# Performance work log

Measured on AMD Instinct MI355X. Metric: run time of the kernel, lower is better.

The kernel has to match this reference:

```python
import jax, jax.numpy as jnp
import numpy as np

ROI = 7      # pooled output size
S = 5        # max adaptive samples per bin dim (boxes <= 0.25*120=30px -> ceil(30/7)=5)


def _roi_align(f, boxes):
    """torchvision roi_align, aligned=True, sampling_ratio=-1 (adaptive).
    f: [C,H,W]; boxes: [N,4] normalized xywh. Returns [N,C,ROI,ROI]."""
    C, H, W = f.shape
    fH, fW = jnp.float32(H), jnp.float32(W)
    x1 = boxes[:, 0] * fW - 0.5                 # aligned=True offset
    y1 = boxes[:, 1] * fH - 0.5
    roi_w = boxes[:, 2] * fW
    roi_h = boxes[:, 3] * fH
    bin_w = roi_w / ROI
    bin_h = roi_h / ROI
    gw = jnp.maximum(jnp.ceil(roi_w / ROI), 1.0)   # adaptive grid counts [N]
    gh = jnp.maximum(jnp.ceil(roi_h / ROI), 1.0)
    ph = jnp.arange(ROI, dtype=jnp.float32)
    s = jnp.arange(S, dtype=jnp.float32)
    # sample coords [N, ROI, S]
    ys = y1[:, None, None] + ph[None, :, None] * bin_h[:, None, None] \
         + (s[None, None, :] + 0.5) * bin_h[:, None, None] / gh[:, None, None]
    xs = x1[:, None, None] + ph[None, :, None] * bin_w[:, None, None] \
         + (s[None, None, :] + 0.5) * bin_w[:, None, None] / gw[:, None, None]
    # broadcast to [N, ROI, ROI, S, S]
    y = ys[:, :, None, :, None]
    x = xs[:, None, :, None, :]
    m = ((s[None, None, None, :, None] < gh[:, None, None, None, None]) &
         (s[None, None, None, None, :] < gw[:, None, None, None, None]))
    valid = (y > -1.0) & (y < fH) & (x > -1.0) & (x < fW)
    yc = jnp.clip(y, 0.0, fH - 1.0)
    xc = jnp.clip(x, 0.0, fW - 1.0)
    y0 = jnp.floor(yc).astype(jnp.int32)
    x0 = jnp.floor(xc).astype(jnp.int32)
    yh = jnp.minimum(y0 + 1, H - 1)
    xh = jnp.minimum(x0 + 1, W - 1)
    ly = yc - y0.astype(jnp.float32); hy = 1.0 - ly
    lx = xc - x0.astype(jnp.float32); hx = 1.0 - lx
    scale = (valid & m).astype(f.dtype)
    y = jnp.broadcast_to(y0 * 0, (boxes.shape[0], ROI, ROI, S, S))  # shape anchor (unused)
    w00 = (hy * hx * scale)[None]
    w01 = (hy * lx * scale)[None]
    w10 = (ly * hx * scale)[None]
    w11 = (ly * lx * scale)[None]
    # gathered values: [C, N, ROI, ROI, S, S]
    vals = (w00 * f[:, y0, x0] + w01 * f[:, y0, xh] +
            w10 * f[:, yh, x0] + w11 * f[:, yh, xh])
    count = (gh * gw)[None, :, None, None]
    pooled = vals.sum(axis=(-1, -2)) / count        # [C, N, ROI, ROI]
    return pooled.transpose(1, 0, 2, 3)              # [N, C, ROI, ROI]


def setup_inputs() -> dict:
    key = jax.random.key(0)
    k = jax.random.split(key, 6)
    features = jax.random.normal(k[0], (1, 128, 120, 120), jnp.float32)
    u = jax.random.uniform(k[1], (512, 4), jnp.float32)
    boxes = jnp.stack([u[:, 0] * 0.7, u[:, 1] * 0.7,
                       0.05 + 0.2 * u[:, 2], 0.05 + 0.2 * u[:, 3]], axis=1)
    d_in = 128 * ROI * ROI  # 6272
    W1 = jax.random.normal(k[2], (d_in, 512), jnp.float32) / np.float32(np.sqrt(d_in))
    b1 = jax.random.normal(k[3], (512,), jnp.float32) * 0.01
    W2 = jax.random.normal(k[4], (512, 256), jnp.float32) / np.float32(np.sqrt(512))
    b2 = jax.random.normal(k[5], (256,), jnp.float32) * 0.01
    return {"features": features, "boxes": boxes, "W1": W1, "b1": b1, "W2": W2, "b2": b2}


def reference(features, boxes, W1, b1, W2, b2):
    roi = _roi_align(features[0], boxes)             # [N,128,7,7]
    flat = roi.reshape(roi.shape[0], -1)             # [N,6272] channel-major like torch .view
    h = jax.nn.relu(flat @ W1 + b1)                  # dropout in eval mode = identity
    return h @ W2 + b2                               # [N,256]
```

## Files before the change

### kernel.cpp

```cpp
#include <hip/hip_runtime.h>
#include <hip/hip_bf16.h>
#include <stdint.h>

#define DI __device__ __forceinline__

typedef __attribute__((ext_vector_type(8))) short short8;
typedef __attribute__((ext_vector_type(4))) float f32x4;

constexpr int CH   = 128;
constexpr int FH   = 120;
constexpr int FW   = 120;
constexpr int NBOX = 512;
constexpr int KDIM = 49 * 128;
constexpr int D1   = 512;
constexpr int D2   = 256;
constexpr int SPLITS = 14;
constexpr int KC     = KDIM / SPLITS;

DI float bf2f(uint32_t u16) { union { uint32_t i; float f; } v; v.i = u16 << 16; return v.f; }
DI uint16_t f2bf(float f) {
    __hip_bfloat16 h = __float2bfloat16(f);
    union { __hip_bfloat16 h; uint16_t u; } v; v.h = h; return v.u;
}

__global__ __launch_bounds__(256) void k_pre(const float* __restrict__ f,
                                             const float* __restrict__ W1,
                                             const float* __restrict__ W2,
                                             uint32_t* __restrict__ ft,
                                             uint16_t* __restrict__ W1rT,
                                             uint16_t* __restrict__ W2T) {
    __shared__ __align__(16) char smem[16896];
    const int v = blockIdx.x, t = threadIdx.x;
    if (v < 480) {
        float* lds = (float*)smem;
        const int y = v >> 2, x0 = (v & 3) * 30;
        for (int e = t; e < 30 * 128; e += 256) {
            int c = e / 30, x = e - c * 30;
            lds[x * 129 + c] = f[c * (FH * FW) + y * FW + x0 + x];
        }
        __syncthreads();
        for (int e = t; e < 30 * 64; e += 256) {
            int x = e >> 6, cp = e & 63;
            float lo = lds[x * 129 + 2 * cp];
            float hi = lds[x * 129 + 2 * cp + 1];
            ft[(y * FW + x0 + x) * 64 + cp] = (uint32_t)f2bf(lo) | ((uint32_t)f2bf(hi) << 16);
        }
    } else if (v < 512) {
        float* lds = (float*)smem;
        const int v2 = v - 480;
        const int n0 = (v2 & 7) * 32, k0 = (v2 >> 3) * 128;
        for (int e = t; e < 4096; e += 256) {
            int k = e >> 5, nn = e & 31;
            lds[k * 33 + nn] = W2[(k0 + k) * D2 + n0 + nn];
        }
        __syncthreads();
        for (int e = t; e < 4096; e += 256) {
            int nn = e >> 7, k = e & 127;
            W2T[(n0 + nn) * D1 + k0 + k] = f2bf(lds[k * 33 + nn]);
        }
    } else {
        float* lds = (float*)smem;
        const int vb = v - 512;
        const int b = vb % 49, j0 = (vb / 49) * 32;
        for (int e = t; e < 4096; e += 256) {
            int ci = e >> 5, jj = e & 31;
            lds[ci * 33 + jj] = W1[(ci * 49 + b) * D1 + j0 + jj];
        }
        __syncthreads();
        for (int e = t; e < 4096; e += 256) {
            int jj = e >> 7, ci = e & 127;
            W1rT[(size_t)(j0 + jj) * KDIM + b * 128 + ci] = f2bf(lds[ci * 33 + jj]);
        }
    }
}

__global__ __launch_bounds__(256) void k_roi(const uint32_t* __restrict__ ft,
                                             const float* __restrict__ boxes,
                                             uint32_t* __restrict__ A) {
#pragma clang fp contract(off)
    const int wid  = (blockIdx.x << 2) + (threadIdx.x >> 6);
    const int lane = threadIdx.x & 63;
    const int box = wid / 49, bin = wid % 49;
    const int ph = bin / 7, pw = bin % 7;

    const float bx = boxes[box * 4 + 0], by = boxes[box * 4 + 1];
    const float bw = boxes[box * 4 + 2], bh = boxes[box * 4 + 3];
    const float x1 = bx * 120.0f - 0.5f;
    const float y1 = by * 120.0f - 0.5f;
    const float roi_w = bw * 120.0f, roi_h = bh * 120.0f;
    const float bin_w = roi_w / 7.0f, bin_h = roi_h / 7.0f;
    const float gwf = fmaxf(ceilf(roi_w / 7.0f), 1.0f);
    const float ghf = fmaxf(ceilf(roi_h / 7.0f), 1.0f);
    const int gwi = (int)gwf, ghi = (int)ghf;

    const float ybase = y1 + (float)ph * bin_h;
    const float xbase = x1 + (float)pw * bin_w;

    float acc0 = 0.0f, acc1 = 0.0f;
    for (int sy = 0; sy < ghi; ++sy) {
        float yy = ybase + ((float)sy + 0.5f) * bin_h / ghf;
        bool vy = (yy > -1.0f) && (yy < 120.0f);
        float yc = fminf(fmaxf(yy, 0.0f), 119.0f);
        int y0 = (int)floorf(yc);
        int yh = min(y0 + 1, 119);
        float ly = yc - (float)y0, hy = 1.0f - ly;
        const uint32_t* r0 = ft + (size_t)(y0 * FW) * 64;
        const uint32_t* r1 = ft + (size_t)(yh * FW) * 64;
        for (int sx = 0; sx < gwi; ++sx) {
            float xx = xbase + ((float)sx + 0.5f) * bin_w / gwf;
            if (!(vy && (xx > -1.0f) && (xx < 120.0f))) continue;
            float xc = fminf(fmaxf(xx, 0.0f), 119.0f);
            int x0 = (int)floorf(xc);
            int xh = min(x0 + 1, 119);
            float lx = xc - (float)x0, hx = 1.0f - lx;
            float w00 = hy * hx, w01 = hy * lx, w10 = ly * hx, w11 = ly * lx;
            uint32_t u00 = r0[x0 * 64 + lane];
            uint32_t u01 = r0[xh * 64 + lane];
            uint32_t u10 = r1[x0 * 64 + lane];
            uint32_t u11 = r1[xh * 64 + lane];
            acc0 += w00 * bf2f(u00 & 0xffffu) + w01 * bf2f(u01 & 0xffffu)
                  + w10 * bf2f(u10 & 0xffffu) + w11 * bf2f(u11 & 0xffffu);
            acc1 += w00 * bf2f(u00 >> 16) + w01 * bf2f(u01 >> 16)
                  + w10 * bf2f(u10 >> 16) + w11 * bf2f(u11 >> 16);
        }
    }
    const float cnt = ghf * gwf;
    const float v0 = acc0 / cnt, v1 = acc1 / cnt;
    A[(size_t)wid * 64 + lane] = (uint32_t)f2bf(v0) | ((uint32_t)f2bf(v1) << 16);
}

__global__ __launch_bounds__(256) void k_gemm1(const uint16_t* __restrict__ A,
                                               const uint16_t* __restrict__ B,
                                               float* __restrict__ P) {
    __shared__ __align__(16) uint16_t As[128 * 32];
    __shared__ __align__(16) uint16_t Bs[128 * 32];
    const int t = threadIdx.x;
    const int lane = t & 63, w = t >> 6;
    const int wr = w >> 1, wc = w & 1;
    const int m0 = blockIdx.x * 128, n0 = blockIdx.y * 128;
    const int kbase = blockIdx.z * KC;

    f32x4 acc[4][4] = {};
    const int kb = lane >> 4, r16 = lane & 15;

    for (int ks = 0; ks < KC / 32; ++ks) {
        const int kk = kbase + ks * 32;
        __syncthreads();
#pragma unroll
        for (int i = 0; i < 2; ++i) {
            int ch = t + 256 * i;
            int row = ch >> 2, c8 = ch & 3;
            int sw = (row >> 1) & 3;
            const uint16_t* ga = A + (size_t)(m0 + row) * KDIM + kk + c8 * 8;
            *(uint4*)&As[row * 32 + (c8 ^ sw) * 8] = *(const uint4*)ga;
            const uint16_t* gb = B + (size_t)(n0 + row) * KDIM + kk + c8 * 8;
            *(uint4*)&Bs[row * 32 + (c8 ^ sw) * 8] = *(const uint4*)gb;
        }
        __syncthreads();

        short8 af[4], bfr[4];
#pragma unroll
        for (int mi = 0; mi < 4; ++mi) {
            int ar = wr * 64 + mi * 16 + r16;
            af[mi] = *(const short8*)&As[ar * 32 + (kb ^ ((ar >> 1) & 3)) * 8];
        }
#pragma unroll
        for (int ni = 0; ni < 4; ++ni) {
            int br = wc * 64 + ni * 16 + r16;
            bfr[ni] = *(const short8*)&Bs[br * 32 + (kb ^ ((br >> 1) & 3)) * 8];
        }
#pragma unroll
        for (int mi = 0; mi < 4; ++mi)
#pragma unroll
            for (int ni = 0; ni < 4; ++ni)
                acc[mi][ni] = __builtin_amdgcn_mfma_f32_16x16x32_bf16(af[mi], bfr[ni], acc[mi][ni], 0, 0, 0);
    }

    float* outp = P + (size_t)blockIdx.z * (D1 * D1);
#pragma unroll
    for (int mi = 0; mi < 4; ++mi)
#pragma unroll
        for (int ni = 0; ni < 4; ++ni) {
            int row = m0 + wr * 64 + mi * 16 + kb * 4;
            int col = n0 + wc * 64 + ni * 16 + r16;
#pragma unroll
            for (int r = 0; r < 4; ++r)
                outp[(size_t)(row + r) * D1 + col] = acc[mi][ni][r];
        }
}

__global__ __launch_bounds__(256) void k_reduce1(const float* __restrict__ P,
                                                 const float* __restrict__ b1,
                                                 uint16_t* __restrict__ Hm) {
    const int e4 = blockIdx.x * 256 + threadIdx.x;
    const f32x4* P4 = (const f32x4*)P;
    f32x4 s = {};
#pragma unroll
    for (int i = 0; i < SPLITS; ++i) s += P4[(size_t)i * (D1 * D1 / 4) + e4];
    const int c4 = (e4 & 127) * 4;
    uint16_t h[4];
#pragma unroll
    for (int j = 0; j < 4; ++j) h[j] = f2bf(fmaxf(s[j] + b1[c4 + j], 0.0f));
    uint2 pk;
    pk.x = (uint32_t)h[0] | ((uint32_t)h[1] << 16);
    pk.y = (uint32_t)h[2] | ((uint32_t)h[3] << 16);
    *(uint2*)&Hm[(size_t)e4 * 4] = pk;
}

__global__ __launch_bounds__(256) void k_gemm2(const uint16_t* __restrict__ Hm,
                                               const uint16_t* __restrict__ W2T,
                                               const float* __restrict__ b2,
                                               float* __restrict__ out) {
    const int wid  = blockIdx.x * 4 + (threadIdx.x >> 6);
    const int lane = threadIdx.x & 63;
    const int mt = wid >> 4, nt = wid & 15;
    const int m0 = mt * 16, n0 = nt * 16;
    const int g = lane >> 4, i = lane & 15;
    f32x4 acc = {};
#pragma unroll
    for (int kk = 0; kk < D1 / 32; ++kk) {
        short8 a = *(const short8*)&Hm[(m0 + i) * D1 + kk * 32 + g * 8];
        short8 b = *(const short8*)&W2T[(n0 + i) * D1 + kk * 32 + g * 8];
        acc = __builtin_amdgcn_mfma_f32_16x16x32_bf16(a, b, acc, 0, 0, 0);
    }
    const float bias = b2[n0 + i];
#pragma unroll
    for (int r = 0; r < 4; ++r)
        out[(size_t)(m0 + g * 4 + r) * D2 + n0 + i] = acc[r] + bias;
}

extern "C" void kernel_launch(void* const* d_in, const int* in_sizes, int n_in,
                              void* d_out, int out_size, void* d_ws, size_t ws_size,
                              hipStream_t stream) {
    const float* f     = (const float*)d_in[0];
    const float* boxes = (const float*)d_in[1];
    const float* W1    = (const float*)d_in[2];
    const float* b1    = (const float*)d_in[3];
    const float* W2    = (const float*)d_in[4];
    const float* b2    = (const float*)d_in[5];
    float* out = (float*)d_out;

    char* p = (char*)d_ws;
    uint32_t* ft   = (uint32_t*)p; p += (size_t)FH * FW * (CH / 2) * 4;
    uint16_t* W1rT = (uint16_t*)p; p += (size_t)D1 * KDIM * 2;
    uint16_t* W2T  = (uint16_t*)p; p += (size_t)D2 * D1 * 2;
    uint16_t* Ar   = (uint16_t*)p; p += (size_t)NBOX * KDIM * 2;
    float*    Pp   = (float*)p;    p += (size_t)SPLITS * D1 * D1 * 4;
    uint16_t* Hm   = (uint16_t*)p; p += (size_t)D1 * D1 * 2;

    k_pre<<<1296, 256, 0, stream>>>(f, W1, W2, ft, W1rT, W2T);
    k_roi<<<(NBOX * 49) / 4, 256, 0, stream>>>(ft, boxes, (uint32_t*)Ar);
    k_gemm1<<<dim3(4, 4, SPLITS), 256, 0, stream>>>(Ar, W1rT, Pp);
    k_reduce1<<<D1 * D1 / 4 / 256, 256, 0, stream>>>(Pp, b1, Hm);
    k_gemm2<<<(D1 / 16) * (D2 / 16) / 4, 256, 0, stream>>>(Hm, W2T, b2, out);
}
```

Before: 72.96 us.

## Replace split-K partial buffers with atomic accumulation and restructure ROI sampling loop

gemm1 now accumulates its split-K partials straight into a single fp32 buffer with relaxed atomics. That buffer is zeroed by extra blocks in the preprocessing kernel. The separate reduce kernel is removed, and bias plus ReLU plus bf16 conversion are folded into gemm2's A-load. The ROI kernel also precomputes per-column x offsets and masked weights, then issues all 20 gathers per row unrolled and branch-free instead of a data-dependent inner loop. This cuts one launch and the 14-way partial-sum write/read traffic, at the cost of atomic contention, nondeterministic summation order, and extra loads for masked-out samples.

After: 81.47 us. 11.7% more time.

```diff
diff --git a/kernel.cpp b/kernel.cpp
--- a/kernel.cpp
+++ b/kernel.cpp
@@ -18,6 +18,7 @@
 constexpr int KC     = KDIM / SPLITS;
 
 DI float bf2f(uint32_t u16) { union { uint32_t i; float f; } v; v.i = u16 << 16; return v.f; }
+DI float bf2f_hi(uint32_t u) { union { uint32_t i; float f; } v; v.i = u & 0xffff0000u; return v.f; }
 DI uint16_t f2bf(float f) {
     __hip_bfloat16 h = __float2bfloat16(f);
     union { __hip_bfloat16 h; uint16_t u; } v; v.h = h; return v.u;
@@ -28,7 +29,8 @@
                                              const float* __restrict__ W2,
                                              uint32_t* __restrict__ ft,
                                              uint16_t* __restrict__ W1rT,
-                                             uint16_t* __restrict__ W2T) {
+                                             uint16_t* __restrict__ W2T,
+                                             float* __restrict__ Hf) {
     __shared__ __align__(16) char smem[16896];
     const int v = blockIdx.x, t = threadIdx.x;
     if (v < 480) {
@@ -58,7 +60,7 @@
             int nn = e >> 7, k = e & 127;
             W2T[(n0 + nn) * D1 + k0 + k] = f2bf(lds[k * 33 + nn]);
         }
-    } else {
+    } else if (v < 1296) {
         float* lds = (float*)smem;
         const int vb = v - 512;
         const int b = vb % 49, j0 = (vb / 49) * 32;
@@ -71,6 +73,11 @@
             int jj = e >> 7, ci = e & 127;
             W1rT[(size_t)(j0 + jj) * KDIM + b * 128 + ci] = f2bf(lds[ci * 33 + jj]);
         }
+    } else {
+        const int vz = v - 1296;
+        f32x4* Z = (f32x4*)(Hf + (size_t)vz * 4096);
+#pragma unroll
+        for (int i = 0; i < 4; ++i) Z[i * 256 + t] = f32x4{0.f, 0.f, 0.f, 0.f};
     }
 }
 
@@ -96,32 +103,48 @@
     const float ybase = y1 + (float)ph * bin_h;
     const float xbase = x1 + (float)pw * bin_w;
 
+    int offx0[5], offxh[5];
+    float hxm[5], lxm[5];
+#pragma unroll
+    for (int j = 0; j < 5; ++j) {
+        float xx = xbase + ((float)j + 0.5f) * bin_w / gwf;
+        bool vx = (j < gwi) && (xx > -1.0f) && (xx < 120.0f);
+        float xc = fminf(fmaxf(xx, 0.0f), 119.0f);
+        int x0 = (int)floorf(xc);
+        int xh = min(x0 + 1, 119);
+        float lx = xc - (float)x0, hx = 1.0f - lx;
+        float mx = vx ? 1.0f : 0.0f;
+        hxm[j] = hx * mx; lxm[j] = lx * mx;
+        offx0[j] = x0 * 64; offxh[j] = xh * 64;
+    }
+
     float acc0 = 0.0f, acc1 = 0.0f;
     for (int sy = 0; sy < ghi; ++sy) {
         float yy = ybase + ((float)sy + 0.5f) * bin_h / ghf;
-        bool vy = (yy > -1.0f) && (yy < 120.0f);
+        float my = ((yy > -1.0f) && (yy < 120.0f)) ? 1.0f : 0.0f;
         float yc = fminf(fmaxf(yy, 0.0f), 119.0f);
         int y0 = (int)floorf(yc);
         int yh = min(y0 + 1, 119);
         float ly = yc - (float)y0, hy = 1.0f - ly;
-        const uint32_t* r0 = ft + (size_t)(y0 * FW) * 64;
-        const uint32_t* r1 = ft + (size_t)(yh * FW) * 64;
-        for (int sx = 0; sx < gwi; ++sx) {
-            float xx = xbase + ((float)sx + 0.5f) * bin_w / gwf;
-            if (!(vy && (xx > -1.0f) && (xx < 120.0f))) continue;
-            float xc = fminf(fmaxf(xx, 0.0f), 119.0f);
-            int x0 = (int)floorf(xc);
-            int xh = min(x0 + 1, 119);
-            float lx = xc - (float)x0, hx = 1.0f - lx;
-            float w00 = hy * hx, w01 = hy * lx, w10 = ly * hx, w11 = ly * lx;
-            uint32_t u00 = r0[x0 * 64 + lane];
-            uint32_t u01 = r0[xh * 64 + lane];
-            uint32_t u10 = r1[x0 * 64 + lane];
-            uint32_t u11 = r1[xh * 64 + lane];
-            acc0 += w00 * bf2f(u00 & 0xffffu) + w01 * bf2f(u01 & 0xffffu)
-                  + w10 * bf2f(u10 & 0xffffu) + w11 * bf2f(u11 & 0xffffu);
-            acc1 += w00 * bf2f(u00 >> 16) + w01 * bf2f(u01 >> 16)
-                  + w10 * bf2f(u10 >> 16) + w11 * bf2f(u11 >> 16);
+        float hym = hy * my, lym = ly * my;
+        const uint32_t* r0 = ft + (size_t)(y0 * FW) * 64 + lane;
+        const uint32_t* r1 = ft + (size_t)(yh * FW) * 64 + lane;
+        uint32_t u00[5], u01[5], u10[5], u11[5];
+#pragma unroll
+        for (int j = 0; j < 5; ++j) {
+            u00[j] = r0[offx0[j]];
+            u01[j] = r0[offxh[j]];
+            u10[j] = r1[offx0[j]];
+            u11[j] = r1[offxh[j]];
+        }
+#pragma unroll
+        for (int j = 0; j < 5; ++j) {
+            float w00 = hym * hxm[j], w01 = hym * lxm[j];
+            float w10 = lym * hxm[j], w11 = lym * lxm[j];
+            acc0 += w00 * bf2f(u00[j] & 0xffffu) + w01 * bf2f(u01[j] & 0xffffu)
+                  + w10 * bf2f(u10[j] & 0xffffu) + w11 * bf2f(u11[j] & 0xffffu);
+            acc1 += w00 * bf2f_hi(u00[j]) + w01 * bf2f_hi(u01[j])
+                  + w10 * bf2f_hi(u10[j]) + w11 * bf2f_hi(u11[j]);
         }
     }
     const float cnt = ghf * gwf;
@@ -131,7 +154,7 @@
 
 __global__ __launch_bounds__(256) void k_gemm1(const uint16_t* __restrict__ A,
                                                const uint16_t* __restrict__ B,
-                                               float* __restrict__ P) {
+                                               float* __restrict__ Hf) {
     __shared__ __align__(16) uint16_t As[128 * 32];
     __shared__ __align__(16) uint16_t Bs[128 * 32];
     const int t = threadIdx.x;
@@ -176,7 +199,6 @@
                 acc[mi][ni] = __builtin_amdgcn_mfma_f32_16x16x32_bf16(af[mi], bfr[ni], acc[mi][ni], 0, 0, 0);
     }
 
-    float* outp = P + (size_t)blockIdx.z * (D1 * D1);
 #pragma unroll
     for (int mi = 0; mi < 4; ++mi)
 #pragma unroll
@@ -185,30 +207,15 @@
             int col = n0 + wc * 64 + ni * 16 + r16;
 #pragma unroll
             for (int r = 0; r < 4; ++r)
-                outp[(size_t)(row + r) * D1 + col] = acc[mi][ni][r];
-        }
-}
-
-__global__ __launch_bounds__(256) void k_reduce1(const float* __restrict__ P,
-                                                 const float* __restrict__ b1,
-                                                 uint16_t* __restrict__ Hm) {
-    const int e4 = blockIdx.x * 256 + threadIdx.x;
-    const f32x4* P4 = (const f32x4*)P;
-    f32x4 s = {};
-#pragma unroll
-    for (int i = 0; i < SPLITS; ++i) s += P4[(size_t)i * (D1 * D1 / 4) + e4];
-    const int c4 = (e4 & 127) * 4;
-    uint16_t h[4];
-#pragma unroll
-    for (int j = 0; j < 4; ++j) h[j] = f2bf(fmaxf(s[j] + b1[c4 + j], 0.0f));
-    uint2 pk;
-    pk.x = (uint32_t)h[0] | ((uint32_t)h[1] << 16);
-    pk.y = (uint32_t)h[2] | ((uint32_t)h[3] << 16);
-    *(uint2*)&Hm[(size_t)e4 * 4] = pk;
-}
-
-__global__ __launch_bounds__(256) void k_gemm2(const uint16_t* __restrict__ Hm,
+                __hip_atomic_fetch_add(&Hf[(size_t)(row + r) * D1 + col],
+                                       acc[mi][ni][r],
+                                       __ATOMIC_RELAXED, __HIP_MEMORY_SCOPE_AGENT);
+        }
+}
+
+__global__ __launch_bounds__(256) void k_gemm2(const float* __restrict__ Hf,
                                                const uint16_t* __restrict__ W2T,
+                                               const float* __restrict__ b1,
                                                const float* __restrict__ b2,
                                                float* __restrict__ out) {
     const int wid  = blockIdx.x * 4 + (threadIdx.x >> 6);
@@ -219,7 +226,18 @@
     f32x4 acc = {};
 #pragma unroll
     for (int kk = 0; kk < D1 / 32; ++kk) {
-        short8 a = *(const short8*)&Hm[(m0 + i) * D1 + kk * 32 + g * 8];
+        const float* hp = &Hf[(size_t)(m0 + i) * D1 + kk * 32 + g * 8];
+        f32x4 h0 = *(const f32x4*)hp;
+        f32x4 h1 = *(const f32x4*)(hp + 4);
+        const float* bp = &b1[kk * 32 + g * 8];
+        f32x4 c0 = *(const f32x4*)bp;
+        f32x4 c1 = *(const f32x4*)(bp + 4);
+        short8 a;
+#pragma unroll
+        for (int r = 0; r < 4; ++r) {
+            a[r]     = (short)f2bf(fmaxf(h0[r] + c0[r], 0.0f));
+            a[4 + r] = (short)f2bf(fmaxf(h1[r] + c1[r], 0.0f));
+        }
         short8 b = *(const short8*)&W2T[(n0 + i) * D1 + kk * 32 + g * 8];
         acc = __builtin_amdgcn_mfma_f32_16x16x32_bf16(a, b, acc, 0, 0, 0);
     }
@@ -245,12 +263,10 @@
     uint16_t* W1rT = (uint16_t*)p; p += (size_t)D1 * KDIM * 2;
     uint16_t* W2T  = (uint16_t*)p; p += (size_t)D2 * D1 * 2;
     uint16_t* Ar   = (uint16_t*)p; p += (size_t)NBOX * KDIM * 2;
-    float*    Pp   = (float*)p;    p += (size_t)SPLITS * D1 * D1 * 4;
-    uint16_t* Hm   = (uint16_t*)p; p += (size_t)D1 * D1 * 2;
-
-    k_pre<<<1296, 256, 0, stream>>>(f, W1, W2, ft, W1rT, W2T);
+    float*    Hf   = (float*)p;    p += (size_t)D1 * D1 * 4;
+
+    k_pre<<<1360, 256, 0, stream>>>(f, W1, W2, ft, W1rT, W2T, Hf);
     k_roi<<<(NBOX * 49) / 4, 256, 0, stream>>>(ft, boxes, (uint32_t*)Ar);
-    k_gemm1<<<dim3(4, 4, SPLITS), 256, 0, stream>>>(Ar, W1rT, Pp);
-    k_reduce1<<<D1 * D1 / 4 / 256, 256, 0, stream>>>(Pp, b1, Hm);
-    k_gemm2<<<(D1 / 16) * (D2 / 16) / 4, 256, 0, stream>>>(Hm, W2T, b2, out);
-}
+    k_gemm1<<<dim3(4, 4, SPLITS), 256, 0, stream>>>(Ar, W1rT, Hf);
+    k_gemm2<<<(D1 / 16) * (D2 / 16) / 4, 256, 0, stream>>>(Hf, W2T, b1, b2, out);
+}
```

## Fuse weight conversion into ROI kernel and precompute per-box sample tables

Applied to the files above, without the earlier changes.

The feature transpose now runs alone in a small pre-kernel. The W1/W2 bf16 transposes move into the ROI kernel as extra blocks, so the weight conversion overlaps with ROI pooling instead of running before it. ROI pooling now uses one 512-thread block per box: it precomputes the y/x sample offsets and bilinear weights into LDS once, and each wave handles bins using those tables. This removes redundant per-bin coordinate math, but block sizes become heterogeneous and the per-box work is less balanced.

New measurement: 91.09 us. 24.9% more time.

```diff
diff --git a/kernel.cpp b/kernel.cpp
--- a/kernel.cpp
+++ b/kernel.cpp
@@ -18,115 +18,135 @@
 constexpr int KC     = KDIM / SPLITS;
 
 DI float bf2f(uint32_t u16) { union { uint32_t i; float f; } v; v.i = u16 << 16; return v.f; }
+DI float bf2f_hi(uint32_t u) { union { uint32_t i; float f; } v; v.i = u & 0xffff0000u; return v.f; }
 DI uint16_t f2bf(float f) {
     __hip_bfloat16 h = __float2bfloat16(f);
     union { __hip_bfloat16 h; uint16_t u; } v; v.h = h; return v.u;
 }
 
-__global__ __launch_bounds__(256) void k_pre(const float* __restrict__ f,
-                                             const float* __restrict__ W1,
-                                             const float* __restrict__ W2,
-                                             uint32_t* __restrict__ ft,
-                                             uint16_t* __restrict__ W1rT,
-                                             uint16_t* __restrict__ W2T) {
-    __shared__ __align__(16) char smem[16896];
+__global__ __launch_bounds__(256) void k_preft(const float* __restrict__ f,
+                                               uint32_t* __restrict__ ft) {
+    __shared__ float lds[30 * 129];
     const int v = blockIdx.x, t = threadIdx.x;
-    if (v < 480) {
-        float* lds = (float*)smem;
-        const int y = v >> 2, x0 = (v & 3) * 30;
-        for (int e = t; e < 30 * 128; e += 256) {
-            int c = e / 30, x = e - c * 30;
-            lds[x * 129 + c] = f[c * (FH * FW) + y * FW + x0 + x];
-        }
-        __syncthreads();
-        for (int e = t; e < 30 * 64; e += 256) {
-            int x = e >> 6, cp = e & 63;
-            float lo = lds[x * 129 + 2 * cp];
-            float hi = lds[x * 129 + 2 * cp + 1];
-            ft[(y * FW + x0 + x) * 64 + cp] = (uint32_t)f2bf(lo) | ((uint32_t)f2bf(hi) << 16);
-        }
-    } else if (v < 512) {
-        float* lds = (float*)smem;
-        const int v2 = v - 480;
-        const int n0 = (v2 & 7) * 32, k0 = (v2 >> 3) * 128;
-        for (int e = t; e < 4096; e += 256) {
-            int k = e >> 5, nn = e & 31;
-            lds[k * 33 + nn] = W2[(k0 + k) * D2 + n0 + nn];
-        }
-        __syncthreads();
-        for (int e = t; e < 4096; e += 256) {
-            int nn = e >> 7, k = e & 127;
-            W2T[(n0 + nn) * D1 + k0 + k] = f2bf(lds[k * 33 + nn]);
-        }
-    } else {
-        float* lds = (float*)smem;
-        const int vb = v - 512;
-        const int b = vb % 49, j0 = (vb / 49) * 32;
-        for (int e = t; e < 4096; e += 256) {
-            int ci = e >> 5, jj = e & 31;
-            lds[ci * 33 + jj] = W1[(ci * 49 + b) * D1 + j0 + jj];
-        }
-        __syncthreads();
-        for (int e = t; e < 4096; e += 256) {
-            int jj = e >> 7, ci = e & 127;
-            W1rT[(size_t)(j0 + jj) * KDIM + b * 128 + ci] = f2bf(lds[ci * 33 + jj]);
-        }
-    }
-}
-
-__global__ __launch_bounds__(256) void k_roi(const uint32_t* __restrict__ ft,
-                                             const float* __restrict__ boxes,
-                                             uint32_t* __restrict__ A) {
+    const int y = v >> 2, x0 = (v & 3) * 30;
+    for (int e = t; e < 30 * 128; e += 256) {
+        int c = e / 30, x = e - c * 30;
+        lds[x * 129 + c] = f[c * (FH * FW) + y * FW + x0 + x];
+    }
+    __syncthreads();
+    for (int e = t; e < 30 * 64; e += 256) {
+        int x = e >> 6, cp = e & 63;
+        float lo = lds[x * 129 + 2 * cp];
+        float hi = lds[x * 129 + 2 * cp + 1];
+        ft[(y * FW + x0 + x) * 64 + cp] = (uint32_t)f2bf(lo) | ((uint32_t)f2bf(hi) << 16);
+    }
+}
+
+__global__ __launch_bounds__(512) void k_roi_w(const uint32_t* __restrict__ ft,
+                                               const float* __restrict__ boxes,
+                                               const float* __restrict__ W1,
+                                               const float* __restrict__ W2,
+                                               uint32_t* __restrict__ A,
+                                               uint16_t* __restrict__ W1rT,
+                                               uint16_t* __restrict__ W2T) {
+    __shared__ __align__(16) float lds[128 * 33];
+    __shared__ float twf[160];
+    __shared__ int   twi[160];
+    const int blk = blockIdx.x, t = threadIdx.x;
+    if (blk < 512) {
 #pragma clang fp contract(off)
-    const int wid  = (blockIdx.x << 2) + (threadIdx.x >> 6);
-    const int lane = threadIdx.x & 63;
-    const int box = wid / 49, bin = wid % 49;
-    const int ph = bin / 7, pw = bin % 7;
-
-    const float bx = boxes[box * 4 + 0], by = boxes[box * 4 + 1];
-    const float bw = boxes[box * 4 + 2], bh = boxes[box * 4 + 3];
-    const float x1 = bx * 120.0f - 0.5f;
-    const float y1 = by * 120.0f - 0.5f;
-    const float roi_w = bw * 120.0f, roi_h = bh * 120.0f;
-    const float bin_w = roi_w / 7.0f, bin_h = roi_h / 7.0f;
-    const float gwf = fmaxf(ceilf(roi_w / 7.0f), 1.0f);
-    const float ghf = fmaxf(ceilf(roi_h / 7.0f), 1.0f);
-    const int gwi = (int)gwf, ghi = (int)ghf;
-
-    const float ybase = y1 + (float)ph * bin_h;
-    const float xbase = x1 + (float)pw * bin_w;
-
-    float acc0 = 0.0f, acc1 = 0.0f;
-    for (int sy = 0; sy < ghi; ++sy) {
-        float yy = ybase + ((float)sy + 0.5f) * bin_h / ghf;
-        bool vy = (yy > -1.0f) && (yy < 120.0f);
-        float yc = fminf(fmaxf(yy, 0.0f), 119.0f);
-        int y0 = (int)floorf(yc);
-        int yh = min(y0 + 1, 119);
-        float ly = yc - (float)y0, hy = 1.0f - ly;
-        const uint32_t* r0 = ft + (size_t)(y0 * FW) * 64;
-        const uint32_t* r1 = ft + (size_t)(yh * FW) * 64;
-        for (int sx = 0; sx < gwi; ++sx) {
-            float xx = xbase + ((float)sx + 0.5f) * bin_w / gwf;
-            if (!(vy && (xx > -1.0f) && (xx < 120.0f))) continue;
+        const int box = blk;
+        const float bx = boxes[box * 4 + 0], by = boxes[box * 4 + 1];
+        const float bw = boxes[box * 4 + 2], bh = boxes[box * 4 + 3];
+        const float x1 = bx * 120.0f - 0.5f;
+        const float y1 = by * 120.0f - 0.5f;
+        const float roi_w = bw * 120.0f, roi_h = bh * 120.0f;
+        const float bin_w = roi_w / 7.0f, bin_h = roi_h / 7.0f;
+        const float gwf = fmaxf(ceilf(roi_w / 7.0f), 1.0f);
+        const float ghf = fmaxf(ceilf(roi_h / 7.0f), 1.0f);
+        const int gwi = (int)gwf, ghi = (int)ghf;
+
+        if (t < 35) {
+            const int ph = t / 5, sy = t % 5;
+            float yy = (y1 + (float)ph * bin_h) + ((float)sy + 0.5f) * bin_h / ghf;
+            float my = ((yy > -1.0f) && (yy < 120.0f)) ? 1.0f : 0.0f;
+            float yc = fminf(fmaxf(yy, 0.0f), 119.0f);
+            int y0 = (int)floorf(yc);
+            int yh = min(y0 + 1, 119);
+            float ly = yc - (float)y0, hy = 1.0f - ly;
+            twf[t]      = hy * my;
+            twf[40 + t] = ly * my;
+            twi[t]      = y0 * (FW * 64);
+            twi[40 + t] = yh * (FW * 64);
+        } else if (t < 70) {
+            const int u = t - 35;
+            const int pw = u / 5, sx = u % 5;
+            float xx = (x1 + (float)pw * bin_w) + ((float)sx + 0.5f) * bin_w / gwf;
+            float mx = ((xx > -1.0f) && (xx < 120.0f)) ? 1.0f : 0.0f;
             float xc = fminf(fmaxf(xx, 0.0f), 119.0f);
             int x0 = (int)floorf(xc);
             int xh = min(x0 + 1, 119);
             float lx = xc - (float)x0, hx = 1.0f - lx;
-            float w00 = hy * hx, w01 = hy * lx, w10 = ly * hx, w11 = ly * lx;
-            uint32_t u00 = r0[x0 * 64 + lane];
-            uint32_t u01 = r0[xh * 64 + lane];
-            uint32_t u10 = r1[x0 * 64 + lane];
-            uint32_t u11 = r1[xh * 64 + lane];
-            acc0 += w00 * bf2f(u00 & 0xffffu) + w01 * bf2f(u01 & 0xffffu)
-                  + w10 * bf2f(u10 & 0xffffu) + w11 * bf2f(u11 & 0xffffu);
-            acc1 += w00 * bf2f(u00 >> 16) + w01 * bf2f(u01 >> 16)
-                  + w10 * bf2f(u10 >> 16) + w11 * bf2f(u11 >> 16);
-        }
-    }
-    const float cnt = ghf * gwf;
-    const float v0 = acc0 / cnt, v1 = acc1 / cnt;
-    A[(size_t)wid * 64 + lane] = (uint32_t)f2bf(v0) | ((uint32_t)f2bf(v1) << 16);
+            twf[80 + u]  = hx * mx;
+            twf[120 + u] = lx * mx;
+            twi[80 + u]  = x0 * 64;
+            twi[120 + u] = xh * 64;
+        }
+        __syncthreads();
+
+        const int w = t >> 6, lane = t & 63;
+        const float cnt = ghf * gwf;
+        for (int bin = w; bin < 49; bin += 8) {
+            const int ph = bin / 7, pw = bin - ph * 7;
+            float acc0 = 0.0f, acc1 = 0.0f;
+            for (int sy = 0; sy < ghi; ++sy) {
+                const int iy = ph * 5 + sy;
+                const float wyh = twf[iy], wyl = twf[40 + iy];
+                const uint32_t* r0 = ft + twi[iy] + lane;
+                const uint32_t* r1 = ft + twi[40 + iy] + lane;
+                for (int sx = 0; sx < gwi; ++sx) {
+                    const int ix = pw * 5 + sx;
+                    const float wxh = twf[80 + ix], wxl = twf[120 + ix];
+                    const int o0 = twi[80 + ix], o1 = twi[120 + ix];
+                    uint32_t u00 = r0[o0], u01 = r0[o1];
+                    uint32_t u10 = r1[o0], u11 = r1[o1];
+                    float w00 = wyh * wxh, w01 = wyh * wxl;
+                    float w10 = wyl * wxh, w11 = wyl * wxl;
+                    acc0 += w00 * bf2f(u00 & 0xffffu) + w01 * bf2f(u01 & 0xffffu)
+                          + w10 * bf2f(u10 & 0xffffu) + w11 * bf2f(u11 & 0xffffu);
+                    acc1 += w00 * bf2f_hi(u00) + w01 * bf2f_hi(u01)
+                          + w10 * bf2f_hi(u10) + w11 * bf2f_hi(u11);
+                }
+            }
+            const float v0 = acc0 / cnt, v1 = acc1 / cnt;
+            A[(size_t)(box * 49 + bin) * 64 + lane] =
+                (uint32_t)f2bf(v0) | ((uint32_t)f2bf(v1) << 16);
+        }
+    } else if (blk < 1296) {
+        const int vb = blk - 512;
+        const int b = vb % 49, j0 = (vb / 49) * 32;
+        for (int e = t; e < 4096; e += 512) {
+            int ci = e >> 5, jj = e & 31;
+            lds[ci * 33 + jj] = W1[(ci * 49 + b) * D1 + j0 + jj];
+        }
+        __syncthreads();
+        for (int e = t; e < 4096; e += 512) {
+            int jj = e >> 7, ci = e & 127;
+            W1rT[(size_t)(j0 + jj) * KDIM + b * 128 + ci] = f2bf(lds[ci * 33 + jj]);
+        }
+    } else {
+        const int v2 = blk - 1296;
+        const int n0 = (v2 & 7) * 32, k0 = (v2 >> 3) * 128;
+        for (int e = t; e < 4096; e += 512) {
+            int k = e >> 5, nn = e & 31;
+            lds[k * 33 + nn] = W2[(k0 + k) * D2 + n0 + nn];
+        }
+        __syncthreads();
+        for (int e = t; e < 4096; e += 512) {
+            int nn = e >> 7, k = e & 127;
+            W2T[(n0 + nn) * D1 + k0 + k] = f2bf(lds[k * 33 + nn]);
+        }
+    }
 }
 
 __global__ __launch_bounds__(256) void k_gemm1(const uint16_t* __restrict__ A,
@@ -248,8 +268,8 @@
     float*    Pp   = (float*)p;    p += (size_t)SPLITS * D1 * D1 * 4;
     uint16_t* Hm   = (uint16_t*)p; p += (size_t)D1 * D1 * 2;
 
-    k_pre<<<1296, 256, 0, stream>>>(f, W1, W2, ft, W1rT, W2T);
-    k_roi<<<(NBOX * 49) / 4, 256, 0, stream>>>(ft, boxes, (uint32_t*)Ar);
+    k_preft<<<480, 256, 0, stream>>>(f, ft);
+    k_roi_w<<<1328, 512, 0, stream>>>(ft, boxes, W1, W2, (uint32_t*)Ar, W1rT, W2T);
     k_gemm1<<<dim3(4, 4, SPLITS), 256, 0, stream>>>(Ar, W1rT, Pp);
     k_reduce1<<<D1 * D1 / 4 / 256, 256, 0, stream>>>(Pp, b1, Hm);
     k_gemm2<<<(D1 / 16) * (D2 / 16) / 4, 256, 0, stream>>>(Hm, W2T, b2, out);
```
